# Kernel optimization log

Measured on AMD Instinct MI355X. Metric: run time of the kernel, lower is better.

Reference implementation:

```python
import jax, jax.numpy as jnp
import numpy as np

N = 50000      # nodes per side
E = 800000     # edges per side
G = 1024       # graphs per batch
VOCAB = 100000
EMB, GH, EH, OUT = 128, 256, 256, 128
HID = GH + EH


def setup_inputs() -> dict:
    key = jax.random.key(0)
    ks = jax.random.split(key, 32)

    def xav(k, shape):
        lim = float(np.sqrt(6.0 / (shape[0] + shape[1])))
        return jax.random.uniform(k, shape, jnp.float32, -lim, lim)

    inp = {
        "x1": jax.random.randint(ks[0], (N,), 0, 11),
        "edge_index1": jax.random.randint(ks[1], (2, E), 0, N),
        "ent1": jax.random.randint(ks[2], (G,), 0, VOCAB),
        "batch1": jnp.sort(jax.random.randint(ks[3], (N,), 0, G)),
        "x2": jax.random.randint(ks[4], (N,), 0, 11),
        "edge_index2": jax.random.randint(ks[5], (2, E), 0, N),
        "ent2": jax.random.randint(ks[6], (G,), 0, VOCAB),
        "batch2": jnp.sort(jax.random.randint(ks[7], (N,), 0, G)),
        # shared GCN params (xavier weights, zero biases as in _reset_params)
        "atom_emb": xav(ks[8], (11, EMB)),
        "gW1": xav(ks[9], (EMB, GH)), "gb1": jnp.zeros((GH,), jnp.float32),
        "gW2": xav(ks[10], (GH, GH)), "gb2": jnp.zeros((GH,), jnp.float32),
        "fcW": xav(ks[11], (GH, GH)), "fcb": jnp.zeros((GH,), jnp.float32),
        # shared entity encoder params
        "ent_emb": xav(ks[12], (VOCAB, EMB)),
        "eW1": xav(ks[13], (EMB, EH)), "eb1": jnp.zeros((EH,), jnp.float32),
        "eW2": xav(ks[14], (EH, EH)), "eb2": jnp.zeros((EH,), jnp.float32),
        # decoder params
        "dW1": xav(ks[15], (HID, HID)), "db1": jnp.zeros((HID,), jnp.float32),
        "dW2": xav(ks[16], (HID, HID)), "db2": jnp.zeros((HID,), jnp.float32),
        "dW3": xav(ks[17], (HID, OUT)), "db3": jnp.zeros((OUT,), jnp.float32),
    }
    return inp


def _gcn_conv(x, W, b, src, dst, n):
    # PyG GCNConv: self-loops + symmetric normalization, out[dst] += norm * (x@W)[src]
    h = x @ W                                   # [n, d_out]
    loop = jnp.arange(n)
    s = jnp.concatenate([src, loop])
    d = jnp.concatenate([dst, loop])
    deg = jax.ops.segment_sum(jnp.ones_like(s, h.dtype), d, num_segments=n)
    dinv = jnp.where(deg > 0, jax.lax.rsqrt(jnp.maximum(deg, 1e-12)), 0.0)
    norm = dinv[s] * dinv[d]                    # [E+n]
    out = jax.ops.segment_sum(h[s] * norm[:, None], d, num_segments=n)
    return out + b


def _gcn_branch(x, edge_index, batch, atom_emb, gW1, gb1, gW2, gb2, fcW, fcb):
    src, dst = edge_index[0], edge_index[1]
    h = atom_emb[x]                             # [N, EMB]
    h = jax.nn.relu(_gcn_conv(h, gW1, gb1, src, dst, N))
    h = jax.nn.relu(_gcn_conv(h, gW2, gb2, src, dst, N))
    # global mean pool per graph
    counts = jax.ops.segment_sum(jnp.ones((N,), h.dtype), batch, num_segments=G)
    pooled = jax.ops.segment_sum(h, batch, num_segments=G) / jnp.maximum(counts, 1.0)[:, None]
    return pooled @ fcW + fcb                   # [G, GH]


def _enc(ent, ent_emb, eW1, eb1, eW2, eb2):
    e = jax.nn.relu(ent_emb[ent])
    e = jax.nn.relu(e @ eW1 + eb1)
    return jax.nn.relu(e @ eW2 + eb2)           # [G, EH]


def reference(x1, edge_index1, ent1, batch1, x2, edge_index2, ent2, batch2,
              atom_emb, gW1, gb1, gW2, gb2, fcW, fcb,
              ent_emb, eW1, eb1, eW2, eb2,
              dW1, db1, dW2, db2, dW3, db3):
    g1 = _gcn_branch(x1, edge_index1, batch1, atom_emb, gW1, gb1, gW2, gb2, fcW, fcb)
    g2 = _gcn_branch(x2, edge_index2, batch2, atom_emb, gW1, gb1, gW2, gb2, fcW, fcb)
    e1 = _enc(ent1, ent_emb, eW1, eb1, eW2, eb2)
    e2 = _enc(ent2, ent_emb, eW1, eb1, eW2, eb2)
    eg1 = jnp.concatenate([g1, e1], axis=1)     # [G, GH+EH]
    eg2 = jnp.concatenate([g2, e2], axis=1)
    egs = jax.nn.relu(eg1 + eg2)
    h = jax.nn.relu(egs @ dW1 + db1)
    h = jax.nn.relu(h @ dW2 + db2)
    return h @ dW3 + db3                        # [G, OUT]
```

## Files before the change

kernel.cpp:

```cpp
#include <hip/hip_runtime.h>
#include <hip/hip_fp16.h>

static constexpr int kN = 50000;
static constexpr int kE = 800000;
static constexpr int kG = 1024;
static constexpr int kEMB = 128;
static constexpr int kGH = 256;
static constexpr int kEH = 256;
static constexpr int kOUT = 128;
static constexpr int kHID = 512;
static constexpr int kNB = (kN + 255) / 256;
static constexpr int kMD = 64;
static constexpr int kNBKT = 196;
static constexpr int kEPB = 3125;
static constexpr int kPBLK = 256;

typedef __attribute__((ext_vector_type(8))) _Float16 half8v;
typedef __attribute__((ext_vector_type(4))) _Float16 half4v;
typedef __attribute__((ext_vector_type(4))) float floatx4;
typedef __attribute__((ext_vector_type(2))) float floatx2;


#define HS_SCALE 128.0f
#define HS_INV   (1.0f / 128.0f)

__device__ inline void acc_fp8x4(unsigned int w, float& a0, float& a1, float& a2, float& a3) {
    floatx2 lo = __builtin_amdgcn_cvt_pk_f32_fp8(w, false);
    floatx2 hi = __builtin_amdgcn_cvt_pk_f32_fp8(w, true);
    a0 += lo[0]; a1 += lo[1]; a2 += hi[0]; a3 += hi[1];
}

__device__ inline float grp16_reduce(float v) {
    int x;
    x = __builtin_amdgcn_update_dpp(0, __float_as_int(v), 0x121, 0xF, 0xF, true);
    v += __int_as_float(x);
    x = __builtin_amdgcn_update_dpp(0, __float_as_int(v), 0x122, 0xF, 0xF, true);
    v += __int_as_float(x);
    x = __builtin_amdgcn_update_dpp(0, __float_as_int(v), 0x124, 0xF, 0xF, true);
    v += __int_as_float(x);
    x = __builtin_amdgcn_update_dpp(0, __float_as_int(v), 0x128, 0xF, 0xF, true);
    v += __int_as_float(x);
    return v;
}

__global__ void prep_kernel(const float* __restrict__ atom_emb, const float* __restrict__ gW1,
                            const float* __restrict__ gW2,
                            float* __restrict__ M11, _Float16* __restrict__ w2t) {
    int i = blockIdx.x * 256 + threadIdx.x;
    if (blockIdx.x < 256) {
        int k = i >> 8, n = i & 255;
        w2t[(size_t)n * kGH + k] = (_Float16)gW2[(size_t)k * kGH + n];
    } else {
        int j = i - 65536;
        if (j < 11 * kGH) {
            int r = j >> 8, c = j & 255;
            float s = 0.f;
            for (int k = 0; k < kEMB; k++) s += atom_emb[r * kEMB + k] * gW1[k * kGH + c];
            M11[j] = s;
        }
    }
}

__global__ void wtrans_kernel(const float* __restrict__ dW1, const float* __restrict__ dW2,
                              const float* __restrict__ dW3, const float* __restrict__ fcW,
                              const float* __restrict__ eW1, const float* __restrict__ eW2,
                              _Float16* __restrict__ dW1t, _Float16* __restrict__ dW2t,
                              _Float16* __restrict__ dW3t, _Float16* __restrict__ fcWt,
                              _Float16* __restrict__ eW1t, _Float16* __restrict__ eW2t) {
    int b = blockIdx.x;
    const float* src; _Float16* dst; int K, N, j0;
    if (b < 1024)      { src = dW1; dst = dW1t; K = 512; N = 512; j0 = b * 256; }
    else if (b < 2048) { src = dW2; dst = dW2t; K = 512; N = 512; j0 = (b - 1024) * 256; }
    else if (b < 2304) { src = dW3; dst = dW3t; K = 512; N = 128; j0 = (b - 2048) * 256; }
    else if (b < 2560) { src = fcW; dst = fcWt; K = 256; N = 256; j0 = (b - 2304) * 256; }
    else if (b < 2688) { src = eW1; dst = eW1t; K = 128; N = 256; j0 = (b - 2560) * 256; }
    else               { src = eW2; dst = eW2t; K = 256; N = 256; j0 = (b - 2688) * 256; }
    int j = j0 + threadIdx.x;
    int n = j / K, k = j - n * K;
    dst[j] = (_Float16)src[(size_t)k * N + n];
}

__global__ void binp1_kernel(const int* __restrict__ ei1, const int* __restrict__ ei2,
                             int* __restrict__ poff) {
    int side = blockIdx.y;
    const int* dst = (side ? ei2 : ei1) + kE;
    __shared__ int hist[kNBKT];
    int t = threadIdx.x;
    if (t < kNBKT) hist[t] = 0;
    __syncthreads();
    int base = blockIdx.x * kEPB;
    for (int j = t; j < kEPB; j += 256)
        atomicAdd(&hist[dst[base + j] >> 8], 1);
    __syncthreads();
    if (t < kNBKT) poff[((side * kNBKT + t) << 8) | blockIdx.x] = hist[t];
}

__global__ void scanA_kernel(int* __restrict__ poff, int* __restrict__ btot) {
    int b = blockIdx.x, side = blockIdx.y, t = threadIdx.x;
    __shared__ int s[256];
    int idx = ((side * kNBKT + b) << 8) | t;
    int v = poff[idx];
    s[t] = v;
    __syncthreads();
    for (int o = 1; o < 256; o <<= 1) {
        int u = (t >= o) ? s[t - o] : 0;
        __syncthreads();
        s[t] += u;
        __syncthreads();
    }
    poff[idx] = s[t] - v;
    if (t == 255) btot[side * kNBKT + b] = s[255];
}

__global__ void scanB_kernel(const int* __restrict__ btot, int* __restrict__ bbase) {
    int side = blockIdx.x, t = threadIdx.x;
    __shared__ int s[256];
    int v = (t < kNBKT) ? btot[side * kNBKT + t] : 0;
    s[t] = v;
    __syncthreads();
    for (int o = 1; o < 256; o <<= 1) {
        int u = (t >= o) ? s[t - o] : 0;
        __syncthreads();
        s[t] += u;
        __syncthreads();
    }
    if (t < kNBKT) bbase[side * (kNBKT + 1) + t] = s[t] - v;
    if (t == 255) bbase[side * (kNBKT + 1) + kNBKT] = s[255];
}

__launch_bounds__(256)
__global__ void binp2_kernel(const int* __restrict__ ei1, const int* __restrict__ ei2,
                             const int* __restrict__ poff, const int* __restrict__ bbase,
                             unsigned int* __restrict__ ebuf) {
    int side = blockIdx.y, blk = blockIdx.x, t = threadIdx.x;
    const int* ei = side ? ei2 : ei1;
    __shared__ int hist[kNBKT], lb[kNBKT], gb[kNBKT], scanbuf[256];
    __shared__ unsigned int sorted[kEPB];
    if (t < kNBKT) hist[t] = 0;
    __syncthreads();
    int base = blk * kEPB;
    for (int j = t; j < kEPB; j += 256)
        atomicAdd(&hist[ei[kE + base + j] >> 8], 1);
    __syncthreads();
    int v = (t < kNBKT) ? hist[t] : 0;
    scanbuf[t] = v;
    __syncthreads();
    for (int o = 1; o < 256; o <<= 1) {
        int u = (t >= o) ? scanbuf[t - o] : 0;
        __syncthreads();
        scanbuf[t] += u;
        __syncthreads();
    }
    if (t < kNBKT) {
        lb[t] = scanbuf[t] - v;
        gb[t] = bbase[side * (kNBKT + 1) + t] + poff[((side * kNBKT + t) << 8) | blk];
        hist[t] = 0;
    }
    __syncthreads();
    for (int j = t; j < kEPB; j += 256) {
        int s_ = ei[base + j];
        int d  = ei[kE + base + j];
        int b  = d >> 8;
        int r  = atomicAdd(&hist[b], 1);
        sorted[lb[b] + r] = ((unsigned int)d << 16) | (unsigned int)s_;
    }
    __syncthreads();
    for (int j = t; j < kEPB; j += 256) {
        unsigned int val = sorted[j];
        int b = val >> 24;
        int gpos = gb[b] + (j - lb[b]);
        ebuf[(size_t)side * kE + gpos] = val;
    }
}

__global__ void binp3_kernel(const unsigned int* __restrict__ ebuf, const int* __restrict__ bbase,
                             unsigned short* __restrict__ col_ell, int* __restrict__ counts,
                             float* __restrict__ dinv, int2* __restrict__ xd,
                             const int* __restrict__ x1, const int* __restrict__ x2) {
    int b = blockIdx.x, side = blockIdx.y, t = threadIdx.x;
    __shared__ int cnt[256];
    cnt[t] = 0;
    __syncthreads();
    int start = bbase[side * (kNBKT + 1) + b];
    int end   = bbase[side * (kNBKT + 1) + b + 1];
    for (int k = start + t; k < end; k += 256) {
        unsigned int v = ebuf[(size_t)side * kE + k];
        int d8 = (v >> 16) & 255;
        int slot = atomicAdd(&cnt[d8], 1);
        if (slot > kMD - 1) slot = kMD - 1;
        int node = (b << 8) | d8;
        col_ell[((size_t)side * kN + node) * kMD + slot] = (unsigned short)(v & 0xFFFFu);
    }
    __syncthreads();
    int node = (b << 8) | t;
    if (node < kN) {
        int d = cnt[t];
        counts[side * kN + node] = d;
        float dv = rsqrtf((float)(d + 1));
        dinv[side * kN + node] = dv;
        const int* x = side ? x2 : x1;
        xd[side * kN + node] = make_int2(x[node], __float_as_int(dv));
    }
}

__global__ void conv1_combine_kernel(const int2* __restrict__ xd,
                                     const int* __restrict__ counts,
                                     const unsigned short* __restrict__ col_ell,
                                     const float* __restrict__ M11,
                                     const float* __restrict__ bias,
                                     _Float16* __restrict__ out) {
    int side = blockIdx.y;
    const int2* xdb = xd + (size_t)side * kN;
    const int* deg = counts + side * kN;
    const unsigned short* ci = col_ell + (size_t)side * kN * kMD;
    _Float16* ob = out + (size_t)side * kN * kGH;

    int tid = threadIdx.x;
    int sub = tid & 15;
    int v = blockIdx.x * 16 + (tid >> 4);

    int cnt = min(deg[v], kMD);
    const unsigned short* cv = ci + (size_t)v * kMD;
    float wt[11];
    #pragma unroll
    for (int t = 0; t < 11; t++) wt[t] = 0.f;
    for (int base = 0; base < cnt; base += 16) {
        int e = base + sub;
        int xs = 15; float ds = 0.f;
        if (e < cnt) {
            int2 t = xdb[(int)cv[e]];
            xs = t.x; ds = __int_as_float(t.y);
        }
        #pragma unroll
        for (int t = 0; t < 11; t++) wt[t] += (xs == t) ? ds : 0.f;
    }
    #pragma unroll
    for (int t = 0; t < 11; t++) wt[t] = grp16_reduce(wt[t]);

    int2 xv = xdb[v];
    float dv = __int_as_float(xv.y);
    #pragma unroll
    for (int q = 0; q < 4; q++) {
        int c = q * 64 + sub * 4;
        float4 bia = *(const float4*)(bias + c);
        float4 m = *(const float4*)(M11 + xv.x * kGH + c);
        float4 acc = make_float4(dv * m.x, dv * m.y, dv * m.z, dv * m.w);
        #pragma unroll
        for (int t = 0; t < 11; t++) {
            float w = wt[t];
            float4 mt = *(const float4*)(M11 + t * kGH + c);
            acc.x += w * mt.x; acc.y += w * mt.y;
            acc.z += w * mt.z; acc.w += w * mt.w;
        }
        half4v o;
        o[0] = (_Float16)fmaxf(dv * acc.x + bia.x, 0.f);
        o[1] = (_Float16)fmaxf(dv * acc.y + bia.y, 0.f);
        o[2] = (_Float16)fmaxf(dv * acc.z + bia.z, 0.f);
        o[3] = (_Float16)fmaxf(dv * acc.w + bia.w, 0.f);
        *(half4v*)(ob + (size_t)v * kGH + c) = o;
    }
}

__launch_bounds__(256)
__global__ void gemm2_mfma_kernel(const _Float16* __restrict__ A,
                                  const _Float16* __restrict__ Bt,
                                  const float* __restrict__ dinv,
                                  unsigned char* __restrict__ C) {
    __shared__ _Float16 As[128][72];
    __shared__ _Float16 Bs[128][72];

    int side = blockIdx.z;
    const _Float16* Ab = A + (size_t)side * kN * kGH;
    const float* db = dinv + (size_t)side * kN;
    unsigned char* Cb = C + (size_t)side * kN * kGH;

    int tid = threadIdx.x;
    int wave = tid >> 6, lane = tid & 63;
    int quad = lane >> 4, r = lane & 15;
    int wm = wave >> 1, wn = wave & 1;
    int row0 = blockIdx.x * 128;
    int col0 = blockIdx.y * 128;

    floatx4 acc[4][4];
    #pragma unroll
    for (int i = 0; i < 4; i++)
        #pragma unroll
        for (int j = 0; j < 4; j++) acc[i][j] = (floatx4){0.f, 0.f, 0.f, 0.f};

    for (int k0 = 0; k0 < kGH; k0 += 64) {
        #pragma unroll
        for (int u = 0; u < 4; u++) {
            int idx = tid + u * 256;
            int row = idx >> 3;
            int seg = (idx & 7) * 8;
            int gr = row0 + row;
            if (gr >= kN) gr = kN - 1;
            *(half8v*)&As[row][seg] = *(const half8v*)(Ab + (size_t)gr * kGH + k0 + seg);
            *(half8v*)&Bs[row][seg] = *(const half8v*)(Bt + (size_t)(col0 + row) * kGH + k0 + seg);
        }
        __syncthreads();
        #pragma unroll
        for (int ks = 0; ks < 2; ks++) {
            half8v af[4], bf[4];
            #pragma unroll
            for (int mt = 0; mt < 4; mt++)
                af[mt] = *(const half8v*)&As[wm * 64 + mt * 16 + r][ks * 32 + quad * 8];
            #pragma unroll
            for (int nt = 0; nt < 4; nt++)
                bf[nt] = *(const half8v*)&Bs[wn * 64 + nt * 16 + r][ks * 32 + quad * 8];
            #pragma unroll
            for (int mt = 0; mt < 4; mt++)
                #pragma unroll
                for (int nt = 0; nt < 4; nt++)
                    acc[mt][nt] = __builtin_amdgcn_mfma_f32_16x16x32_f16(af[mt], bf[nt],
                                                                         acc[mt][nt], 0, 0, 0);
        }
        __syncthreads();
    }

    #pragma unroll
    for (int mt = 0; mt < 4; mt++) {
        #pragma unroll
        for (int i = 0; i < 4; i++) {
            int grow = row0 + wm * 64 + mt * 16 + quad * 4 + i;
            if (grow >= kN) continue;
            float rsq = db[grow] * HS_SCALE;
            #pragma unroll
            for (int nt = 0; nt < 4; nt++) {
                int gcol = col0 + wn * 64 + nt * 16 + r;
                float q = acc[mt][nt][i] * rsq;
                Cb[(size_t)grow * kGH + gcol] =
                    (unsigned char)__builtin_amdgcn_cvt_pk_fp8_f32(q, q, 0, false);
            }
        }
    }
}

__launch_bounds__(256)
__global__ void gemm_tail_kernel(const _Float16* __restrict__ A,
                                 const _Float16* __restrict__ Bt,
                                 void* __restrict__ Cout,
                                 int N, int K,
                                 const float* __restrict__ bias,
                                 int relu, int f32out) {
    __shared__ _Float16 As[64][72];
    __shared__ _Float16 Bs[64][72];
    int tid = threadIdx.x;
    int wave = tid >> 6, lane = tid & 63;
    int quad = lane >> 4, r = lane & 15;
    int wm = wave >> 1, wn = wave & 1;
    int row0 = blockIdx.x * 64, col0 = blockIdx.y * 64;

    floatx4 acc[2][2];
    #pragma unroll
    for (int i = 0; i < 2; i++)
        #pragma unroll
        for (int j = 0; j < 2; j++) acc[i][j] = (floatx4){0.f, 0.f, 0.f, 0.f};

    for (int k0 = 0; k0 < K; k0 += 64) {
        #pragma unroll
        for (int u = 0; u < 2; u++) {
            int idx = tid + u * 256;
            int row = idx >> 3;
            int seg = (idx & 7) * 8;
            *(half8v*)&As[row][seg] = *(const half8v*)(A + (size_t)(row0 + row) * K + k0 + seg);
            *(half8v*)&Bs[row][seg] = *(const half8v*)(Bt + (size_t)(col0 + row) * K + k0 + seg);
        }
        __syncthreads();
        #pragma unroll
        for (int ks = 0; ks < 2; ks++) {
            half8v af[2], bf[2];
            #pragma unroll
            for (int mt = 0; mt < 2; mt++)
                af[mt] = *(const half8v*)&As[wm * 32 + mt * 16 + r][ks * 32 + quad * 8];
            #pragma unroll
            for (int nt = 0; nt < 2; nt++)
                bf[nt] = *(const half8v*)&Bs[wn * 32 + nt * 16 + r][ks * 32 + quad * 8];
            #pragma unroll
            for (int mt = 0; mt < 2; mt++)
                #pragma unroll
                for (int nt = 0; nt < 2; nt++)
                    acc[mt][nt] = __builtin_amdgcn_mfma_f32_16x16x32_f16(af[mt], bf[nt],
                                                                         acc[mt][nt], 0, 0, 0);
        }
        __syncthreads();
    }

    #pragma unroll
    for (int mt = 0; mt < 2; mt++) {
        #pragma unroll
        for (int i = 0; i < 4; i++) {
            int grow = row0 + wm * 32 + mt * 16 + quad * 4 + i;
            #pragma unroll
            for (int nt = 0; nt < 2; nt++) {
                int gcol = col0 + wn * 32 + nt * 16 + r;
                float v = acc[mt][nt][i] + bias[gcol];
                if (relu) v = fmaxf(v, 0.f);
                if (f32out) ((float*)Cout)[(size_t)grow * N + gcol] = v;
                else ((_Float16*)Cout)[(size_t)grow * N + gcol] = (_Float16)v;
            }
        }
    }
}

__global__ void aggpool_kernel(const unsigned char* __restrict__ hs, const float* __restrict__ dinv,
                               const int* __restrict__ counts,
                               const unsigned short* __restrict__ col_ell,
                               const float* __restrict__ bias,
                               const int* __restrict__ batch1, const int* __restrict__ batch2,
                               _Float16* __restrict__ pooled16) {
    int side = blockIdx.y;
    int g = blockIdx.x;
    const unsigned char* hb = hs + (size_t)side * kN * kGH;
    const float* dv_ = dinv + side * kN;
    const int* deg = counts + side * kN;
    const unsigned short* ci = col_ell + (size_t)side * kN * kMD;
    const int* batch = side ? batch2 : batch1;

    int lo = 0, hi = kN;
    while (lo < hi) { int mid = (lo + hi) >> 1; if (batch[mid] < g) lo = mid + 1; else hi = mid; }
    int start = lo;
    lo = start; hi = kN;
    while (lo < hi) { int mid = (lo + hi) >> 1; if (batch[mid] < g + 1) lo = mid + 1; else hi = mid; }
    int end = lo;

    int wave = threadIdx.x >> 6;
    int lane = threadIdx.x & 63;
    int c = lane * 4;
    float4 bia = *(const float4*)(bias + c);
    float p0 = 0.f, p1 = 0.f, p2 = 0.f, p3 = 0.f;

    for (int v = start + wave; v < end; v += 4) {
        float dv = dv_[v];
        float a0 = 0.f, a1 = 0.f, a2 = 0.f, a3 = 0.f;
        acc_fp8x4(*(const unsigned int*)(hb + (size_t)v * kGH + c), a0, a1, a2, a3);
        int cnt = min(deg[v], kMD);
        int idxl = (lane < cnt) ? (int)ci[(size_t)v * kMD + lane] : 0;
        int j = 0;
        for (; j + 16 <= cnt; j += 16) {
            unsigned int w[16];
            #pragma unroll
            for (int u = 0; u < 16; u++)
                w[u] = *(const unsigned int*)(hb + (size_t)__shfl(idxl, j + u) * kGH + c);
            #pragma unroll
            for (int u = 0; u < 16; u++) acc_fp8x4(w[u], a0, a1, a2, a3);
        }
        for (; j + 8 <= cnt; j += 8) {
            unsigned int w[8];
            #pragma unroll
            for (int u = 0; u < 8; u++)
                w[u] = *(const unsigned int*)(hb + (size_t)__shfl(idxl, j + u) * kGH + c);
            #pragma unroll
            for (int u = 0; u < 8; u++) acc_fp8x4(w[u], a0, a1, a2, a3);
        }
        for (; j < cnt; j++)
            acc_fp8x4(*(const unsigned int*)(hb + (size_t)__shfl(idxl, j) * kGH + c),
                      a0, a1, a2, a3);
        float f = dv * HS_INV;
        p0 += fmaxf(f * a0 + bia.x, 0.f);
        p1 += fmaxf(f * a1 + bia.y, 0.f);
        p2 += fmaxf(f * a2 + bia.z, 0.f);
        p3 += fmaxf(f * a3 + bia.w, 0.f);
    }

    __shared__ float psum[4][256];
    *(float4*)&psum[wave][c] = make_float4(p0, p1, p2, p3);
    __syncthreads();
    int t = threadIdx.x;
    if (t < 256) {
        float s = psum[0][t] + psum[1][t] + psum[2][t] + psum[3][t];
        float inv = 1.0f / fmaxf((float)(end - start), 1.0f);
        pooled16[(size_t)(side * kG + g) * kGH + t] = (_Float16)(s * inv);
    }
}

__global__ void egather_kernel(const float* __restrict__ emb,
                               const int* __restrict__ ent1, const int* __restrict__ ent2,
                               _Float16* __restrict__ e16) {
    int rr = blockIdx.x;
    int idx = (rr < kG) ? ent1[rr] : ent2[rr - kG];
    int k = threadIdx.x;
    e16[(size_t)rr * kEMB + k] = (_Float16)fmaxf(emb[(size_t)idx * kEMB + k], 0.f);
}

__global__ void egsprep_kernel(const _Float16* __restrict__ gfc16,
                               const _Float16* __restrict__ ento16,
                               _Float16* __restrict__ egs16) {
    int idx = blockIdx.x * 256 + threadIdx.x;
    int g = idx >> 6;
    int k8 = (idx & 63) * 8;
    const _Float16* src = (k8 < kGH) ? gfc16 : ento16;
    int kk = (k8 < kGH) ? k8 : k8 - kGH;
    half8v a = *(const half8v*)(src + (size_t)g * kGH + kk);
    half8v b = *(const half8v*)(src + (size_t)(g + kG) * kGH + kk);
    half8v o;
    #pragma unroll
    for (int u = 0; u < 8; u++) o[u] = (_Float16)fmaxf((float)a[u] + (float)b[u], 0.f);
    *(half8v*)(egs16 + (size_t)g * kHID + k8) = o;
}

static inline char* carve(char*& p, size_t bytes) {
    char* r = p;
    p += (bytes + 255) & ~(size_t)255;
    return r;
}

extern "C" void kernel_launch(void* const* d_in, const int* in_sizes, int n_in,
                              void* d_out, int out_size, void* d_ws, size_t ws_size,
                              hipStream_t stream) {
    const int*   x1       = (const int*)d_in[0];
    const int*   ei1      = (const int*)d_in[1];
    const int*   ent1     = (const int*)d_in[2];
    const int*   batch1   = (const int*)d_in[3];
    const int*   x2       = (const int*)d_in[4];
    const int*   ei2      = (const int*)d_in[5];
    const int*   ent2     = (const int*)d_in[6];
    const int*   batch2   = (const int*)d_in[7];
    const float* atom_emb = (const float*)d_in[8];
    const float* gW1      = (const float*)d_in[9];
    const float* gb1      = (const float*)d_in[10];
    const float* gW2      = (const float*)d_in[11];
    const float* gb2      = (const float*)d_in[12];
    const float* fcW      = (const float*)d_in[13];
    const float* fcb      = (const float*)d_in[14];
    const float* ent_emb  = (const float*)d_in[15];
    const float* eW1      = (const float*)d_in[16];
    const float* eb1      = (const float*)d_in[17];
    const float* eW2      = (const float*)d_in[18];
    const float* eb2      = (const float*)d_in[19];
    const float* dW1      = (const float*)d_in[20];
    const float* db1      = (const float*)d_in[21];
    const float* dW2      = (const float*)d_in[22];
    const float* db2      = (const float*)d_in[23];
    const float* dW3      = (const float*)d_in[24];
    const float* db3      = (const float*)d_in[25];
    float* out = (float*)d_out;

    char* p = (char*)d_ws;
    _Float16* h2_h   = (_Float16*)carve(p, (size_t)2 * kN * kGH * 2);
    unsigned char* hs8 = (unsigned char*)carve(p, (size_t)2 * kN * kGH);
    unsigned short* col_ell = (unsigned short*)carve(p, (size_t)2 * kN * kMD * 2);
    unsigned int* ebuf = (unsigned int*)carve(p, (size_t)2 * kE * 4);
    int*   poff    = (int*)  carve(p, (size_t)2 * kNBKT * 256 * 4);
    int*   btot    = (int*)  carve(p, (size_t)2 * kNBKT * 4);
    int*   bbase   = (int*)  carve(p, (size_t)2 * (kNBKT + 1) * 4);
    int*   counts  = (int*)  carve(p, (size_t)2 * kN * 4);
    float* dinv    = (float*)carve(p, (size_t)2 * kN * 4);
    int2*  xd      = (int2*) carve(p, (size_t)2 * kN * 8);
    float* M11     = (float*)carve(p, 11 * kGH * 4);
    _Float16* w2t  = (_Float16*)carve(p, (size_t)kGH * kGH * 2);
    _Float16* pooled16 = (_Float16*)carve(p, (size_t)2 * kG * kGH * 2);
    _Float16* gfc16    = (_Float16*)carve(p, (size_t)2 * kG * kGH * 2);
    _Float16* e16      = (_Float16*)carve(p, (size_t)2 * kG * kEMB * 2);
    _Float16* etmp16   = (_Float16*)carve(p, (size_t)2 * kG * kEH * 2);
    _Float16* ento16   = (_Float16*)carve(p, (size_t)2 * kG * kEH * 2);
    _Float16* egs16    = (_Float16*)carve(p, (size_t)kG * kHID * 2);
    _Float16* dh1_16   = (_Float16*)carve(p, (size_t)kG * kHID * 2);
    _Float16* dh2_16   = (_Float16*)carve(p, (size_t)kG * kHID * 2);
    _Float16* dW1t = (_Float16*)carve(p, (size_t)kHID * kHID * 2);
    _Float16* dW2t = (_Float16*)carve(p, (size_t)kHID * kHID * 2);
    _Float16* dW3t = (_Float16*)carve(p, (size_t)kOUT * kHID * 2);
    _Float16* fcWt = (_Float16*)carve(p, (size_t)kGH * kGH * 2);
    _Float16* eW1t = (_Float16*)carve(p, (size_t)kEH * kEMB * 2);
    _Float16* eW2t = (_Float16*)carve(p, (size_t)kEH * kEH * 2);

    prep_kernel<<<267, 256, 0, stream>>>(atom_emb, gW1, gW2, M11, w2t);
    wtrans_kernel<<<2944, 256, 0, stream>>>(dW1, dW2, dW3, fcW, eW1, eW2,
                                            dW1t, dW2t, dW3t, fcWt, eW1t, eW2t);
    binp1_kernel<<<dim3(kPBLK, 2), 256, 0, stream>>>(ei1, ei2, poff);
    scanA_kernel<<<dim3(kNBKT, 2), 256, 0, stream>>>(poff, btot);
    scanB_kernel<<<2, 256, 0, stream>>>(btot, bbase);
    binp2_kernel<<<dim3(kPBLK, 2), 256, 0, stream>>>(ei1, ei2, poff, bbase, ebuf);
    binp3_kernel<<<dim3(kNBKT, 2), 256, 0, stream>>>(ebuf, bbase, col_ell, counts,
                                                     dinv, xd, x1, x2);
    conv1_combine_kernel<<<dim3(kN / 16, 2), 256, 0, stream>>>(xd, counts, col_ell,
                                                               M11, gb1, h2_h);

    gemm2_mfma_kernel<<<dim3((kN + 127) / 128, kGH / 128, 2), 256, 0, stream>>>(h2_h, w2t,
                                                                                dinv, hs8);
    aggpool_kernel<<<dim3(kG, 2), 256, 0, stream>>>(hs8, dinv, counts, col_ell,
                                                    gb2, batch1, batch2, pooled16);
    egather_kernel<<<2 * kG, 128, 0, stream>>>(ent_emb, ent1, ent2, e16);

    gemm_tail_kernel<<<dim3(2 * kG / 64, kGH / 64), 256, 0, stream>>>(
        pooled16, fcWt, gfc16, kGH, kGH, fcb, 0, 0);
    gemm_tail_kernel<<<dim3(2 * kG / 64, kEH / 64), 256, 0, stream>>>(
        e16, eW1t, etmp16, kEH, kEMB, eb1, 1, 0);
    gemm_tail_kernel<<<dim3(2 * kG / 64, kEH / 64), 256, 0, stream>>>(
        etmp16, eW2t, ento16, kEH, kEH, eb2, 1, 0);
    egsprep_kernel<<<kG * kHID / 8 / 256, 256, 0, stream>>>(gfc16, ento16, egs16);
    gemm_tail_kernel<<<dim3(kG / 64, kHID / 64), 256, 0, stream>>>(
        egs16, dW1t, dh1_16, kHID, kHID, db1, 1, 0);
    gemm_tail_kernel<<<dim3(kG / 64, kHID / 64), 256, 0, stream>>>(
        dh1_16, dW2t, dh2_16, kHID, kHID, db2, 1, 0);
    gemm_tail_kernel<<<dim3(kG / 64, kOUT / 64), 256, 0, stream>>>(
        dh2_16, dW3t, out, kOUT, kHID, db3, 0, 1);
}
```

Baseline: 428.9 us.

## Split per-graph aggregation-pool across multiple blocks with a separate partial-sum reduction

The fused aggregate-and-mean-pool kernel is split so each graph is processed by eight blocks, each taking an interleaved subset of the graph's nodes and writing float partial sums to a workspace buffer. A new reduction kernel then sums the partials and divides by the node count to produce pooled fp16 output. This raises the grid from about 2K to about 16K blocks, giving the gather-heavy aggregation more parallelism and latency hiding for graphs of only ~49 nodes. The cost is an extra launch, an extra workspace buffer with its write/read traffic, and repeated binary searches in every block.

Result: slower. 457.2 us (+6.6%).

```diff
diff --git a/kernel.cpp b/kernel.cpp
--- a/kernel.cpp
+++ b/kernel.cpp
@@ -14,6 +14,7 @@
 static constexpr int kNBKT = 196;
 static constexpr int kEPB = 3125;
 static constexpr int kPBLK = 256;
+static constexpr int kPP = 8;
 
 typedef __attribute__((ext_vector_type(8))) _Float16 half8v;
 typedef __attribute__((ext_vector_type(4))) _Float16 half4v;
@@ -403,14 +404,15 @@
     }
 }
 
-__global__ void aggpool_kernel(const unsigned char* __restrict__ hs, const float* __restrict__ dinv,
-                               const int* __restrict__ counts,
-                               const unsigned short* __restrict__ col_ell,
-                               const float* __restrict__ bias,
-                               const int* __restrict__ batch1, const int* __restrict__ batch2,
-                               _Float16* __restrict__ pooled16) {
+__global__ void aggpoolp_kernel(const unsigned char* __restrict__ hs, const float* __restrict__ dinv,
+                                const int* __restrict__ counts,
+                                const unsigned short* __restrict__ col_ell,
+                                const float* __restrict__ bias,
+                                const int* __restrict__ batch1, const int* __restrict__ batch2,
+                                float* __restrict__ ppart) {
     int side = blockIdx.y;
-    int g = blockIdx.x;
+    int g = blockIdx.x / kPP;
+    int pI = blockIdx.x - g * kPP;
     const unsigned char* hb = hs + (size_t)side * kN * kGH;
     const float* dv_ = dinv + side * kN;
     const int* deg = counts + side * kN;
@@ -430,7 +432,7 @@
     float4 bia = *(const float4*)(bias + c);
     float p0 = 0.f, p1 = 0.f, p2 = 0.f, p3 = 0.f;
 
-    for (int v = start + wave; v < end; v += 4) {
+    for (int v = start + pI * 4 + wave; v < end; v += 4 * kPP) {
         float dv = dv_[v];
         float a0 = 0.f, a1 = 0.f, a2 = 0.f, a3 = 0.f;
         acc_fp8x4(*(const unsigned int*)(hb + (size_t)v * kGH + c), a0, a1, a2, a3);
@@ -467,11 +469,29 @@
     *(float4*)&psum[wave][c] = make_float4(p0, p1, p2, p3);
     __syncthreads();
     int t = threadIdx.x;
-    if (t < 256) {
-        float s = psum[0][t] + psum[1][t] + psum[2][t] + psum[3][t];
-        float inv = 1.0f / fmaxf((float)(end - start), 1.0f);
-        pooled16[(size_t)(side * kG + g) * kGH + t] = (_Float16)(s * inv);
-    }
+    float s = psum[0][t] + psum[1][t] + psum[2][t] + psum[3][t];
+    ppart[(((size_t)side * kG + g) * kPP + pI) * kGH + t] = s;
+}
+
+__global__ void preduce_kernel(const float* __restrict__ ppart,
+                               const int* __restrict__ batch1, const int* __restrict__ batch2,
+                               _Float16* __restrict__ pooled16) {
+    int side = blockIdx.y;
+    int g = blockIdx.x;
+    const int* batch = side ? batch2 : batch1;
+    int lo = 0, hi = kN;
+    while (lo < hi) { int mid = (lo + hi) >> 1; if (batch[mid] < g) lo = mid + 1; else hi = mid; }
+    int start = lo;
+    lo = start; hi = kN;
+    while (lo < hi) { int mid = (lo + hi) >> 1; if (batch[mid] < g + 1) lo = mid + 1; else hi = mid; }
+    int end = lo;
+    int t = threadIdx.x;
+    const float* pb = ppart + (((size_t)side * kG + g) * kPP) * kGH;
+    float s = 0.f;
+    #pragma unroll
+    for (int p = 0; p < kPP; p++) s += pb[p * kGH + t];
+    float inv = 1.0f / fmaxf((float)(end - start), 1.0f);
+    pooled16[(size_t)(side * kG + g) * kGH + t] = (_Float16)(s * inv);
 }
 
 __global__ void egather_kernel(const float* __restrict__ emb,
@@ -549,6 +569,7 @@
     int2*  xd      = (int2*) carve(p, (size_t)2 * kN * 8);
     float* M11     = (float*)carve(p, 11 * kGH * 4);
     _Float16* w2t  = (_Float16*)carve(p, (size_t)kGH * kGH * 2);
+    float* ppart   = (float*)carve(p, (size_t)2 * kG * kPP * kGH * 4);
     _Float16* pooled16 = (_Float16*)carve(p, (size_t)2 * kG * kGH * 2);
     _Float16* gfc16    = (_Float16*)carve(p, (size_t)2 * kG * kGH * 2);
     _Float16* e16      = (_Float16*)carve(p, (size_t)2 * kG * kEMB * 2);
@@ -578,8 +599,9 @@
 
     gemm2_mfma_kernel<<<dim3((kN + 127) / 128, kGH / 128, 2), 256, 0, stream>>>(h2_h, w2t,
                                                                                 dinv, hs8);
-    aggpool_kernel<<<dim3(kG, 2), 256, 0, stream>>>(hs8, dinv, counts, col_ell,
-                                                    gb2, batch1, batch2, pooled16);
+    aggpoolp_kernel<<<dim3(kG * kPP, 2), 256, 0, stream>>>(hs8, dinv, counts, col_ell,
+                                                           gb2, batch1, batch2, ppart);
+    preduce_kernel<<<dim3(kG, 2), 256, 0, stream>>>(ppart, batch1, batch2, pooled16);
     egather_kernel<<<2 * kG, 128, 0, stream>>>(ent_emb, ent1, ent2, e16);
 
     gemm_tail_kernel<<<dim3(2 * kG / 64, kGH / 64), 256, 0, stream>>>(
```
